# Kernel tuning notes

Hardware: AMD Instinct MI355X
Metric: run time of the kernel (lower is better)

The kernel has to match this reference:

```python
import jax, jax.numpy as jnp
import numpy as np

B, S, N = 16, 512, 321          # batch, input length, n_variates (dec_in)
D, DF, LAYERS = 512, 2048, 2    # d_model, d_ff, e_layers
M, K, P = 3, 3, 96              # wavelet levels, kernel_size, pred_len
ALPHA = 0.3


def _dwconv(x, h, dilation):
    # x: [B, C, L], h: [C, K] depthwise dilated conv (cross-correlation, like torch)
    return jax.lax.conv_general_dilated(
        x, h[:, None, :], window_strides=(1,), padding='VALID',
        rhs_dilation=(dilation,), dimension_numbers=('NCH', 'OIH', 'NCH'),
        feature_group_count=x.shape[1])


def _swt_dec(x, h0, h1):
    # stationary wavelet decomposition; x: [B, N, D] -> [B, N, M+1, D]
    approx, coeffs, dil = x, [], 1
    for _ in range(M):
        pad_total = dil * (K - 1)
        pad_r = (K * dil) // 2
        xp = jnp.pad(approx, ((0, 0), (0, 0), (pad_total - pad_r, pad_r)), mode='wrap')
        coeffs.append(_dwconv(xp, h1, dil))
        approx = _dwconv(xp, h0, dil)
        dil *= 2
    coeffs.append(approx)
    return jnp.stack(coeffs[::-1], axis=-2)


def _swt_rec(c, g0, g1):
    # inverse SWT; c: [B, N, M+1, D] -> [B, N, D]
    approx = c[:, :, 0, :]
    dil = 2 ** (M - 1)
    for i in range(M):
        det = c[:, :, 1 + i, :]
        pad_total = dil * (K - 1)
        pad_l = (dil * K) // 2
        pads = ((0, 0), (0, 0), (pad_l, pad_total - pad_l))
        approx = (_dwconv(jnp.pad(approx, pads, mode='wrap'), g0, dil)
                  + _dwconv(jnp.pad(det, pads, mode='wrap'), g1, dil)) / 2
        dil //= 2
    return approx


def _geom_attention(q, k, v):
    # q,k,v: [B, L=D, H=M+1, E=N]
    scale = 1.0 / jnp.sqrt(jnp.float32(q.shape[-1]))
    dot = jnp.einsum('blhe,bshe->bhls', q, k)
    qn2 = jnp.sum(q * q, -1).transpose(0, 2, 1)  # [B,H,L]
    kn2 = jnp.sum(k * k, -1).transpose(0, 2, 1)  # [B,H,S]
    wedge = jnp.sqrt(jax.nn.relu(qn2[:, :, :, None] * kn2[:, :, None, :] - dot * dot) + 1e-8)
    scores = ((1.0 - ALPHA) * dot + ALPHA * wedge) * scale
    A = jax.nn.softmax(scores, axis=-1)
    return jnp.einsum('bhls,bshd->blhd', A, v)


def _layernorm(x, g, b, eps=1e-5):
    mu = x.mean(-1, keepdims=True)
    var = jnp.mean((x - mu) ** 2, -1, keepdims=True)
    return (x - mu) / jnp.sqrt(var + eps) * g + b


def _forward(x_enc, emb_W, emb_b, h0, h1, g0, g1, Wq, bq, Wk, bk, Wv, bv, Wo, bo,
             W1, b1, W2, b2, ln1_g, ln1_b, ln2_g, ln2_b, lnf_g, lnf_b, proj_W, proj_b):
    # RevIN-style normalize (means detached as in torch code)
    means = jax.lax.stop_gradient(x_enc.mean(1, keepdims=True))
    stdev = jnp.sqrt(x_enc.var(1, keepdims=True) + 1e-5)
    x = (x_enc - means) / stdev
    # inverted embedding: each variate's full series -> d_model token
    h = jnp.einsum('bsn,ds->bnd', x, emb_W) + emb_b  # [B,N,D]
    for l in range(LAYERS):
        coeffs = _swt_dec(h, h0[l], h1[l])  # [B,N,M+1,D]
        q = (jnp.einsum('bnmd,ed->bnme', coeffs, Wq[l]) + bq[l]).transpose(0, 3, 2, 1)
        kk = (jnp.einsum('bnmd,ed->bnme', coeffs, Wk[l]) + bk[l]).transpose(0, 3, 2, 1)
        vv = (jnp.einsum('bnmd,ed->bnme', coeffs, Wv[l]) + bv[l]).transpose(0, 3, 2, 1)
        out = _geom_attention(q, kk, vv).transpose(0, 3, 2, 1)  # [B,N,M+1,D]
        out = _swt_rec(out, g0[l], g1[l])                        # [B,N,D]
        out = jnp.einsum('bnd,ed->bne', out, Wo[l]) + bo[l]
        x1 = _layernorm(h + out, ln1_g[l], ln1_b[l])
        y = jax.nn.gelu(jnp.einsum('bnd,fd->bnf', x1, W1[l]) + b1[l], approximate=False)
        y = jnp.einsum('bnf,df->bnd', y, W2[l]) + b2[l]
        h = _layernorm(x1 + y, ln2_g[l], ln2_b[l])
    h = _layernorm(h, lnf_g, lnf_b)
    dec = (jnp.einsum('bnd,pd->bnp', h, proj_W) + proj_b).transpose(0, 2, 1)  # [B,P,N]
    dec = dec * stdev[:, 0, :][:, None, :] + means[:, 0, :][:, None, :]
    return dec, means, stdev


def setup_inputs():
    key = jax.random.key(0)
    ks = jax.random.split(key, 24)
    def filt(k):
        f = jax.random.normal(k, (LAYERS, N, K), jnp.float32)
        return f / jnp.linalg.norm(f, axis=-1, keepdims=True)
    w = lambda k, shape: jax.random.normal(k, shape, jnp.float32) * 0.02
    z = lambda shape: jnp.zeros(shape, jnp.float32)
    o = lambda shape: jnp.ones(shape, jnp.float32)
    return {
        'x_enc': jax.random.normal(ks[0], (B, S, N), jnp.float32),
        'emb_W': w(ks[1], (D, S)), 'emb_b': z((D,)),
        'h0': filt(ks[2]), 'h1': filt(ks[3]), 'g0': filt(ks[4]), 'g1': filt(ks[5]),
        'Wq': w(ks[6], (LAYERS, D, D)), 'bq': z((LAYERS, D)),
        'Wk': w(ks[7], (LAYERS, D, D)), 'bk': z((LAYERS, D)),
        'Wv': w(ks[8], (LAYERS, D, D)), 'bv': z((LAYERS, D)),
        'Wo': w(ks[9], (LAYERS, D, D)), 'bo': z((LAYERS, D)),
        'W1': w(ks[10], (LAYERS, DF, D)), 'b1': z((LAYERS, DF)),
        'W2': w(ks[11], (LAYERS, D, DF)), 'b2': z((LAYERS, D)),
        'ln1_g': o((LAYERS, D)), 'ln1_b': z((LAYERS, D)),
        'ln2_g': o((LAYERS, D)), 'ln2_b': z((LAYERS, D)),
        'lnf_g': o((D,)), 'lnf_b': z((D,)),
        'proj_W': w(ks[12], (P, D)), 'proj_b': z((P,)),
    }


def reference(x_enc, emb_W, emb_b, h0, h1, g0, g1, Wq, bq, Wk, bk, Wv, bv, Wo, bo,
              W1, b1, W2, b2, ln1_g, ln1_b, ln2_g, ln2_b, lnf_g, lnf_b, proj_W, proj_b):
    return _forward(x_enc, emb_W, emb_b, h0, h1, g0, g1, Wq, bq, Wk, bk, Wv, bv, Wo, bo,
                    W1, b1, W2, b2, ln1_g, ln1_b, ln2_g, ln2_b, lnf_g, lnf_b, proj_W, proj_b)
```

## Files before the change

kernel.cpp:

```cpp
#include <hip/hip_runtime.h>
#include <hip/hip_bf16.h>
#include <math.h>
#include <stdint.h>

#define Bn 16
#define Sn 512
#define Nn 321
#define Dn 512
#define DFn 2048
#define Pn 96
#define KP 352

typedef __bf16 bf16x8 __attribute__((ext_vector_type(8)));
typedef float f32x4 __attribute__((ext_vector_type(4)));
typedef __hip_bfloat16 bf16;

static __device__ __forceinline__ float gelu_exact(float x) {
    return 0.5f * x * (1.0f + erff(x * 0.7071067811865476f));
}

static __device__ __forceinline__ void gld16(const void* g, void* l) {
    __builtin_amdgcn_global_load_lds(
        (const __attribute__((address_space(1))) void*)(uintptr_t)g,
        (__attribute__((address_space(3))) void*)(uintptr_t)l, 16, 0, 0);
}

struct CvtPack {
    const float* src[14];
    bf16* dst[14];
    int cnt[14];
};
__global__ void cvt_all_kernel(CvtPack p) {
    int seg = blockIdx.y;
    int n = p.cnt[seg];
    const float* s = p.src[seg];
    bf16* d = p.dst[seg];
    int i = (blockIdx.x * 256 + threadIdx.x) * 4;
    if (i + 3 < n) {
        float4 v = *reinterpret_cast<const float4*>(s + i);
        d[i] = __float2bfloat16(v.x);
        d[i + 1] = __float2bfloat16(v.y);
        d[i + 2] = __float2bfloat16(v.z);
        d[i + 3] = __float2bfloat16(v.w);
    }
}

__global__ void bias_pack_kernel(const float* __restrict__ bq, const float* __restrict__ bk,
                                 float* __restrict__ bqk) {
    int idx = blockIdx.x * 256 + threadIdx.x;
    if (idx >= 2048) return;
    int l = idx >> 10, j = idx & 1023;
    bqk[idx] = (j < 512) ? bq[l * 512 + j] : bk[l * 512 + j - 512];
}

__global__ void stats_kernel(const float* __restrict__ x, float* __restrict__ means,
                             float* __restrict__ stdev) {
    int b = blockIdx.y;
    int n = blockIdx.x * 256 + threadIdx.x;
    if (n >= Nn) return;
    const float* p = x + (size_t)b * Sn * Nn + n;
    float s = 0.f, s2 = 0.f;
    for (int ss = 0; ss < Sn; ++ss) { float v = p[(size_t)ss * Nn]; s += v; s2 += v * v; }
    float mu = s * (1.0f / Sn);
    float var = s2 * (1.0f / Sn) - mu * mu;
    means[b * Nn + n] = mu;
    stdev[b * Nn + n] = sqrtf(var + 1e-5f);
}

__global__ void transpose_norm_kernel(const float* __restrict__ x,
                                      const float* __restrict__ means,
                                      const float* __restrict__ stdev,
                                      bf16* __restrict__ xT) {
    __shared__ float tile[32][33];
    int b = blockIdx.z;
    int s0 = blockIdx.x * 32, n0 = blockIdx.y * 32;
    int tx = threadIdx.x, ty = threadIdx.y;
#pragma unroll
    for (int u = 0; u < 4; ++u) {
        int srow = ty + u * 8;
        int n = n0 + tx;
        tile[srow][tx] = (n < Nn) ? x[((size_t)b * Sn + (s0 + srow)) * Nn + n] : 0.f;
    }
    __syncthreads();
#pragma unroll
    for (int u = 0; u < 4; ++u) {
        int n = n0 + ty + u * 8;
        int s = s0 + tx;
        if (n < Nn) {
            float mu = means[b * Nn + n], sd = stdev[b * Nn + n];
            xT[((size_t)b * Nn + n) * Sn + s] = __float2bfloat16((tile[tx][ty + u * 8] - mu) / sd);
        }
    }
}

template <int OUT, int EPI>
__global__ __launch_bounds__(256) void mm_kernel(
    const bf16* __restrict__ A, const bf16* __restrict__ Bm,
    const float* __restrict__ bias, void* __restrict__ C,
    int Mdim, int Ndim, int Kdim, int lda, int ldb, int ldc,
    long sAi, long sAo, long sBi, long sBo, long sCi, long sCo, int innerB) {
    int z = blockIdx.z;
    int zi = z % innerB, zo = z / innerB;
    const bf16* Ab = A + (size_t)zi * sAi + (size_t)zo * sAo;
    const bf16* Bb = Bm + (size_t)zi * sBi + (size_t)zo * sBo;

    int gx = gridDim.x, gy = gridDim.y;
    int lin = blockIdx.y * gx + blockIdx.x;
    int prefix = (gy & ~7) * gx;
    int bx, by;
    if (lin < prefix) {
        bx = (lin >> 3) % gx;
        by = (lin / (8 * gx)) * 8 + (lin & 7);
    } else {
        int r = lin - prefix;
        bx = r % gx;
        by = (gy & ~7) + r / gx;
    }

    __shared__ __align__(16) bf16 As[2][128 * 32];
    __shared__ __align__(16) bf16 Bs[2][128 * 32];
    int t = threadIdx.x;
    int wave = t >> 6, lane = t & 63;
    int wr = wave >> 1, wc = wave & 1;
    int q = lane >> 4, l16 = lane & 15;
    int i0 = by * 128, j0 = bx * 128;

    int srow0 = t >> 2;
    int scol = (t & 3) * 8;
    f32x4 acc[4][4] = {};

    int nIter = Kdim >> 5;

    auto stage = [&](int k0, int buf) {
#pragma unroll
        for (int u = 0; u < 2; ++u) {
            int row = u * 64 + srow0;
            int gcol = scol ^ (((row >> 1) & 3) << 3);
            int gi = i0 + row; if (gi >= Mdim) gi = Mdim - 1;
            gld16(Ab + (size_t)gi * lda + k0 + gcol, &As[buf][u * 2048 + wave * 512]);
            int gj = j0 + row; if (gj >= Ndim) gj = Ndim - 1;
            gld16(Bb + (size_t)gj * ldb + k0 + gcol, &Bs[buf][u * 2048 + wave * 512]);
        }
    };

    stage(0, 0);
    for (int it = 0; it < nIter; ++it) {
        __syncthreads();
        if (it + 1 < nIter) stage((it + 1) << 5, (it + 1) & 1);
        int buf = it & 1;
        bf16x8 af[4], bfr[4];
#pragma unroll
        for (int mi = 0; mi < 4; ++mi) {
            int r = wr * 64 + mi * 16 + l16;
            int cl = (q * 8) ^ (((r >> 1) & 3) << 3);
            af[mi] = *reinterpret_cast<const bf16x8*>(&As[buf][r * 32 + cl]);
        }
#pragma unroll
        for (int ni = 0; ni < 4; ++ni) {
            int r = wc * 64 + ni * 16 + l16;
            int cl = (q * 8) ^ (((r >> 1) & 3) << 3);
            bfr[ni] = *reinterpret_cast<const bf16x8*>(&Bs[buf][r * 32 + cl]);
        }
#pragma unroll
        for (int mi = 0; mi < 4; ++mi)
#pragma unroll
            for (int ni = 0; ni < 4; ++ni)
                acc[mi][ni] = __builtin_amdgcn_mfma_f32_16x16x32_bf16(af[mi], bfr[ni], acc[mi][ni], 0, 0, 0);
    }
    size_t cbase = (size_t)zi * sCi + (size_t)zo * sCo;
#pragma unroll
    for (int mi = 0; mi < 4; ++mi) {
#pragma unroll
        for (int r = 0; r < 4; ++r) {
            int gi = i0 + wr * 64 + mi * 16 + q * 4 + r;
            if (gi >= Mdim) continue;
#pragma unroll
            for (int ni = 0; ni < 4; ++ni) {
                int gj = j0 + wc * 64 + ni * 16 + l16;
                if (gj >= Ndim) continue;
                float v = acc[mi][ni][r];
                if (bias) v += bias[gj];
                if (EPI == 1) v = gelu_exact(v);
                size_t cidx = cbase + (size_t)gi * ldc + gj;
                if (OUT == 0) ((float*)C)[cidx] = v;
                else ((bf16*)C)[cidx] = __float2bfloat16(v);
            }
        }
    }
}

__global__ __launch_bounds__(128) void swt_dec_kernel(
    const float* __restrict__ h, const float* __restrict__ h0f,
    const float* __restrict__ h1f, bf16* __restrict__ coeffs) {
    __shared__ float a[2][512];
    int b = blockIdx.y, n = blockIdx.x, t = threadIdx.x;
    const float* hrow = h + ((size_t)b * Nn + n) * Dn;
#pragma unroll
    for (int u = 0; u < 4; ++u) a[0][t + u * 128] = hrow[t + u * 128];
    float f0[3], f1[3];
#pragma unroll
    for (int k = 0; k < 3; ++k) { f0[k] = h0f[n * 3 + k]; f1[k] = h1f[n * 3 + k]; }
    __syncthreads();
    bf16* cb = coeffs + ((size_t)b * Nn + n) * 4 * Dn;
    int cur = 0;
    for (int lev = 0; lev < 3; ++lev) {
        int dil = 1 << lev;
        int pl = 2 * dil - (3 * dil) / 2;
#pragma unroll
        for (int u = 0; u < 4; ++u) {
            int d = t + u * 128;
            float dv = 0.f, av = 0.f;
#pragma unroll
            for (int k = 0; k < 3; ++k) {
                int idx = (d + k * dil - pl) & 511;
                float xv = a[cur][idx];
                dv += f1[k] * xv;
                av += f0[k] * xv;
            }
            cb[(size_t)(3 - lev) * Dn + d] = __float2bfloat16(dv);
            a[cur ^ 1][d] = av;
        }
        __syncthreads();
        cur ^= 1;
    }
#pragma unroll
    for (int u = 0; u < 4; ++u) cb[t + u * 128] = __float2bfloat16(a[cur][t + u * 128]);
}

__global__ __launch_bounds__(128) void swt_rec_kernel(
    const bf16* __restrict__ attn, const float* __restrict__ g0f,
    const float* __restrict__ g1f, bf16* __restrict__ rec) {
    __shared__ float a[2][512];
    __shared__ float det[512];
    int b = blockIdx.y, n = blockIdx.x, t = threadIdx.x;
    const bf16* base = attn + ((size_t)(b * 4) * Nn + n) * Dn;
#pragma unroll
    for (int u = 0; u < 4; ++u) a[0][t + u * 128] = __bfloat162float(base[t + u * 128]);
    float w0[3], w1[3];
#pragma unroll
    for (int k = 0; k < 3; ++k) { w0[k] = g0f[n * 3 + k]; w1[k] = g1f[n * 3 + k]; }
    int cur = 0;
    for (int i = 0; i < 3; ++i) {
        int dil = 4 >> i;
        int pl = (3 * dil) / 2;
        const bf16* drow = base + (size_t)(1 + i) * Nn * Dn;
#pragma unroll
        for (int u = 0; u < 4; ++u) det[t + u * 128] = __bfloat162float(drow[t + u * 128]);
        __syncthreads();
#pragma unroll
        for (int u = 0; u < 4; ++u) {
            int d = t + u * 128;
            float s = 0.f;
#pragma unroll
            for (int k = 0; k < 3; ++k) {
                int idx = (d + k * dil - pl) & 511;
                s += w0[k] * a[cur][idx] + w1[k] * det[idx];
            }
            a[cur ^ 1][d] = s * 0.5f;
        }
        __syncthreads();
        cur ^= 1;
    }
    bf16* out = rec + ((size_t)b * Nn + n) * Dn;
#pragma unroll
    for (int u = 0; u < 4; ++u) out[t + u * 128] = __float2bfloat16(a[cur][t + u * 128]);
}

__global__ void tconv2_kernel(const bf16* __restrict__ QK, bf16* __restrict__ QtKt) {
    __shared__ bf16 tile[32][33];
    int zz = blockIdx.z;
    int qk = zz >> 6, bm = zz & 63;
    int b = bm >> 2, m = bm & 3;
    int e0 = blockIdx.x * 32, n0 = blockIdx.y * 32;
    int tx = threadIdx.x, ty = threadIdx.y;
    const bf16* ib = QK + (size_t)b * Nn * 4096 + (size_t)m * 1024 + (size_t)qk * 512;
    bf16* ob = QtKt + (size_t)qk * 64 * 512 * KP + (size_t)bm * 512 * KP;
#pragma unroll
    for (int u = 0; u < 4; ++u) {
        int n = n0 + ty + u * 8;
        bf16 v = __float2bfloat16(0.f);
        if (n < Nn) v = ib[(size_t)n * 4096 + e0 + tx];
        tile[ty + u * 8][tx] = v;
    }
    __syncthreads();
#pragma unroll
    for (int u = 0; u < 4; ++u) {
        int e = e0 + ty + u * 8;
        int n = n0 + tx;
        if (n < KP) ob[(size_t)e * KP + n] = tile[tx][ty + u * 8];
    }
}

__global__ __launch_bounds__(256) void colsq_t_kernel(const bf16* __restrict__ QtKt,
                                                      float* __restrict__ outv) {
    int wave = threadIdx.x >> 6, lane = threadIdx.x & 63;
    size_t row = (size_t)blockIdx.x * 4 + wave;
    const bf16* p = QtKt + row * KP;
    float s = 0.f;
#pragma unroll
    for (int j = 0; j < 6; ++j) {
        int idx = lane + j * 64;
        if (idx < KP) { float v = __bfloat162float(p[idx]); s += v * v; }
    }
#pragma unroll
    for (int m = 1; m < 64; m <<= 1) s += __shfl_xor(s, m);
    if (lane == 0) outv[row] = s;
}

__global__ __launch_bounds__(256) void wedge_softmax_kernel(
    bf16* __restrict__ Smat, const float* __restrict__ qn2, const float* __restrict__ kn2) {
    int wave = threadIdx.x >> 6, lane = threadIdx.x & 63;
    int rowid = blockIdx.x * 4 + wave;
    int bm = rowid >> 9, l = rowid & 511;
    bf16* row = Smat + (size_t)rowid * 512;
    const float* kn = kn2 + (size_t)bm * 512;
    float q2 = qn2[(size_t)bm * 512 + l];
    const float scale = rsqrtf(321.0f);
    bf16x8 dv = *reinterpret_cast<const bf16x8*>(row + lane * 8);
    float kk[8];
    *reinterpret_cast<float4*>(&kk[0]) = *reinterpret_cast<const float4*>(kn + lane * 8);
    *reinterpret_cast<float4*>(&kk[4]) = *reinterpret_cast<const float4*>(kn + lane * 8 + 4);
    float sc[8];
    float mx = -1e30f;
#pragma unroll
    for (int j = 0; j < 8; ++j) {
        float d = (float)dv[j];
        float w = sqrtf(fmaxf(q2 * kk[j] - d * d, 0.f) + 1e-8f);
        sc[j] = (0.7f * d + 0.3f * w) * scale;
        mx = fmaxf(mx, sc[j]);
    }
#pragma unroll
    for (int m = 1; m < 64; m <<= 1) mx = fmaxf(mx, __shfl_xor(mx, m));
    float sum = 0.f;
#pragma unroll
    for (int j = 0; j < 8; ++j) { sc[j] = expf(sc[j] - mx); sum += sc[j]; }
#pragma unroll
    for (int m = 1; m < 64; m <<= 1) sum += __shfl_xor(sum, m);
    float inv = 1.0f / sum;
    bf16x8 o;
#pragma unroll
    for (int j = 0; j < 8; ++j) o[j] = (__bf16)(sc[j] * inv);
    *reinterpret_cast<bf16x8*>(row + lane * 8) = o;
}

__global__ __launch_bounds__(256) void ln_kernel(
    const float* __restrict__ A, const float* __restrict__ R, const float* __restrict__ R2,
    const float* __restrict__ g, const float* __restrict__ bb,
    float* __restrict__ outf, bf16* __restrict__ outb) {
    int wave = threadIdx.x >> 6, lane = threadIdx.x & 63;
    size_t r = (size_t)blockIdx.x * 4 + wave;
    const float* ra = A + r * Dn + lane * 8;
    float x[8];
    *reinterpret_cast<float4*>(&x[0]) = *reinterpret_cast<const float4*>(ra);
    *reinterpret_cast<float4*>(&x[4]) = *reinterpret_cast<const float4*>(ra + 4);
    if (R) {
        const float* rr = R + r * Dn + lane * 8;
        float y[8];
        *reinterpret_cast<float4*>(&y[0]) = *reinterpret_cast<const float4*>(rr);
        *reinterpret_cast<float4*>(&y[4]) = *reinterpret_cast<const float4*>(rr + 4);
#pragma unroll
        for (int j = 0; j < 8; ++j) x[j] += y[j];
    }
    if (R2) {
        const float* rr = R2 + r * Dn + lane * 8;
        float y[8];
        *reinterpret_cast<float4*>(&y[0]) = *reinterpret_cast<const float4*>(rr);
        *reinterpret_cast<float4*>(&y[4]) = *reinterpret_cast<const float4*>(rr + 4);
#pragma unroll
        for (int j = 0; j < 8; ++j) x[j] += y[j];
    }
    float s = 0.f, s2 = 0.f;
#pragma unroll
    for (int j = 0; j < 8; ++j) { s += x[j]; s2 += x[j] * x[j]; }
#pragma unroll
    for (int m = 1; m < 64; m <<= 1) { s += __shfl_xor(s, m); s2 += __shfl_xor(s2, m); }
    float mean = s * (1.0f / Dn);
    float var = s2 * (1.0f / Dn) - mean * mean;
    float inv = rsqrtf(var + 1e-5f);
#pragma unroll
    for (int j = 0; j < 8; ++j) {
        int d = lane * 8 + j;
        float v = (x[j] - mean) * inv * g[d] + bb[d];
        if (outf) outf[r * Dn + d] = v;
        if (outb) outb[r * Dn + d] = __float2bfloat16(v);
    }
}

__global__ void out_scale_kernel(const float* __restrict__ ptmp,
                                 const float* __restrict__ means,
                                 const float* __restrict__ stdev, float* __restrict__ dec) {
    int idx = blockIdx.x * 256 + threadIdx.x;
    if (idx >= Bn * Pn * Nn) return;
    int n = idx % Nn;
    int bp = idx / Nn;
    int p = bp % Pn;
    int b = bp / Pn;
    const size_t PS = (size_t)Bn * Nn * Pn;
    size_t base = ((size_t)b * Nn + n) * Pn + p;
    float v = ptmp[base] + ptmp[base + PS] + ptmp[base + 2 * PS] + ptmp[base + 3 * PS];
    dec[idx] = v * stdev[b * Nn + n] + means[b * Nn + n];
}

extern "C" void kernel_launch(void* const* d_in, const int* in_sizes, int n_in,
                              void* d_out, int out_size, void* d_ws, size_t ws_size,
                              hipStream_t stream) {
    const float* x_enc = (const float*)d_in[0];
    const float* emb_W = (const float*)d_in[1];
    const float* emb_b = (const float*)d_in[2];
    const float* h0 = (const float*)d_in[3];
    const float* h1 = (const float*)d_in[4];
    const float* g0 = (const float*)d_in[5];
    const float* g1 = (const float*)d_in[6];
    const float* Wq = (const float*)d_in[7];
    const float* bq = (const float*)d_in[8];
    const float* Wk = (const float*)d_in[9];
    const float* bk = (const float*)d_in[10];
    const float* Wv = (const float*)d_in[11];
    const float* bv = (const float*)d_in[12];
    const float* Wo = (const float*)d_in[13];
    const float* bo = (const float*)d_in[14];
    const float* W1 = (const float*)d_in[15];
    const float* b1 = (const float*)d_in[16];
    const float* W2 = (const float*)d_in[17];
    const float* b2 = (const float*)d_in[18];
    const float* ln1_g = (const float*)d_in[19];
    const float* ln1_b = (const float*)d_in[20];
    const float* ln2_g = (const float*)d_in[21];
    const float* ln2_b = (const float*)d_in[22];
    const float* lnf_g = (const float*)d_in[23];
    const float* lnf_b = (const float*)d_in[24];
    const float* proj_W = (const float*)d_in[25];
    const float* proj_b = (const float*)d_in[26];

    float* dec = (float*)d_out;
    float* means = dec + (size_t)Bn * Pn * Nn;
    float* stdev = means + (size_t)Bn * Nn;

    char* p = (char*)d_ws;
    auto alloc = [&](size_t bytes) { char* r = p; p += (bytes + 255) & ~(size_t)255; return r; };
    const size_t RD = (size_t)Bn * Nn * Dn;
    const size_t RQ4 = RD * 4;

    bf16* embWb = (bf16*)alloc(262144 * 2);
    bf16* Wqkb = (bf16*)alloc(2 * 524288 * 2);
    bf16* Wvb = (bf16*)alloc(2 * 262144 * 2);
    bf16* Wob = (bf16*)alloc(2 * 262144 * 2);
    bf16* W1b = (bf16*)alloc(2 * 1048576 * 2);
    bf16* W2b = (bf16*)alloc(2 * 1048576 * 2);
    bf16* projWb = (bf16*)alloc(49152 * 2);
    float* bqk = (float*)alloc(2048 * 4);

    float* hbuf = (float*)alloc(RD * 4);
    char* regC = alloc(RQ4 * 2);
    char* regQ = alloc(RQ4 * 2);
    char* regK = alloc(RQ4 * 2);
    char* regV = alloc(RQ4 * 2);
    char* regT = alloc((size_t)2 * 64 * 512 * KP * 2);
    float* qn2 = (float*)alloc((size_t)2 * 64 * 512 * 4);
    float* kn2 = qn2 + 32768;

    bf16* coeffs_b = (bf16*)regC;
    bf16* attn_b = (bf16*)regC;
    bf16* QK0b = (bf16*)regQ;
    bf16* Smat = (bf16*)regQ;
    bf16* recb = (bf16*)regQ;
    bf16* x1b = (bf16*)(regQ + RD * 2);
    float* ptmp = (float*)regQ;
    bf16* V0b = (bf16*)regV;
    bf16* yb = (bf16*)regV;
    bf16* QtKt = (bf16*)regT;
    bf16* Qt = QtKt;
    bf16* Kt = QtKt + (size_t)64 * 512 * KP;
    bf16* xT_b = (bf16*)regT;
    float* x1 = (float*)regT;
    float* tmp = (float*)(regT + RD * 4);
    bf16* hfb = (bf16*)(regT + RD * 12);

    const int R = Bn * Nn;
    const int RQr = R * 4;
    const long sbm = (long)4 * Nn * 512;
    const long sS = (long)512 * 512;
    const long sTq = (long)512 * KP;
    const long sTb = 4 * sTq;

    CvtPack cp;
    int ci = 0;
    auto addcvt = [&](const float* s, bf16* d, int n) { cp.src[ci] = s; cp.dst[ci] = d; cp.cnt[ci] = n; ++ci; };
    addcvt(emb_W, embWb, 262144);
    for (int l = 0; l < 2; ++l) {
        addcvt(Wq + (size_t)l * 262144, Wqkb + (size_t)l * 524288, 262144);
        addcvt(Wk + (size_t)l * 262144, Wqkb + (size_t)l * 524288 + 262144, 262144);
        addcvt(Wv + (size_t)l * 262144, Wvb + (size_t)l * 262144, 262144);
        addcvt(Wo + (size_t)l * 262144, Wob + (size_t)l * 262144, 262144);
        addcvt(W1 + (size_t)l * 1048576, W1b + (size_t)l * 1048576, 1048576);
        addcvt(W2 + (size_t)l * 1048576, W2b + (size_t)l * 1048576, 1048576);
    }
    addcvt(proj_W, projWb, 49152);
    cvt_all_kernel<<<dim3(1048576 / 4 / 256, 14), 256, 0, stream>>>(cp);
    bias_pack_kernel<<<8, 256, 0, stream>>>(bq, bk, bqk);

    stats_kernel<<<dim3((Nn + 255) / 256, Bn), 256, 0, stream>>>(x_enc, means, stdev);
    transpose_norm_kernel<<<dim3(Sn / 32, (Nn + 31) / 32, Bn), dim3(32, 8), 0, stream>>>(
        x_enc, means, stdev, xT_b);

    mm_kernel<0, 0><<<dim3(4, (R + 127) / 128, 1), 256, 0, stream>>>(
        xT_b, embWb, emb_b, hbuf, R, Dn, Sn, Sn, Sn, Dn, 0, 0, 0, 0, 0, 0, 1);

    for (int l = 0; l < 2; ++l) {
        const float* h0l = h0 + (size_t)l * Nn * 3;
        const float* h1l = h1 + (size_t)l * Nn * 3;
        const float* g0l = g0 + (size_t)l * Nn * 3;
        const float* g1l = g1 + (size_t)l * Nn * 3;

        swt_dec_kernel<<<dim3(Nn, Bn), 128, 0, stream>>>(hbuf, h0l, h1l, coeffs_b);

        mm_kernel<1, 0><<<dim3(8, (RQr + 127) / 128, 1), 256, 0, stream>>>(
            coeffs_b, Wqkb + (size_t)l * 524288, bqk + (size_t)l * 1024, QK0b,
            RQr, 1024, Dn, Dn, Dn, 1024, 0, 0, 0, 0, 0, 0, 1);
        mm_kernel<1, 0><<<dim3(4, (RQr + 127) / 128, 1), 256, 0, stream>>>(
            coeffs_b, Wvb + (size_t)l * 262144, bv + (size_t)l * Dn, V0b,
            RQr, Dn, Dn, Dn, Dn, Dn, 0, 0, 0, 0, 0, 0, 1);

        tconv2_kernel<<<dim3(16, 11, 128), dim3(32, 8), 0, stream>>>(QK0b, QtKt);
        colsq_t_kernel<<<16384, 256, 0, stream>>>(QtKt, qn2);

        mm_kernel<1, 0><<<dim3(4, 4, 64), 256, 0, stream>>>(
            Qt, Kt, nullptr, Smat, 512, 512, KP, KP, KP, 512,
            sTq, sTb, sTq, sTb, sS, 4 * sS, 4);

        wedge_softmax_kernel<<<8192, 256, 0, stream>>>(Smat, qn2, kn2);

        mm_kernel<1, 0><<<dim3(4, (Nn + 127) / 128, 64), 256, 0, stream>>>(
            V0b, Smat, nullptr, attn_b, Nn, 512, 512, 2048, 512, 512,
            512, sbm, sS, 4 * sS, (long)Nn * 512, (long)4 * Nn * 512, 4);

        swt_rec_kernel<<<dim3(Nn, Bn), 128, 0, stream>>>(attn_b, g0l, g1l, recb);

        mm_kernel<0, 0><<<dim3(4, (R + 127) / 128, 2), 256, 0, stream>>>(
            recb, Wob + (size_t)l * 262144, bo + (size_t)l * Dn, tmp,
            R, Dn, 256, Dn, Dn, Dn, 256, 0, 256, 0, (long)RD, 0, 2);
        ln_kernel<<<R / 4, 256, 0, stream>>>(hbuf, tmp, tmp + RD, ln1_g + (size_t)l * Dn,
                                             ln1_b + (size_t)l * Dn, x1, x1b);

        mm_kernel<1, 1><<<dim3(16, (R + 127) / 128, 1), 256, 0, stream>>>(
            x1b, W1b + (size_t)l * 1048576, b1 + (size_t)l * DFn, yb,
            R, DFn, Dn, Dn, Dn, DFn, 0, 0, 0, 0, 0, 0, 1);
        mm_kernel<0, 0><<<dim3(4, (R + 127) / 128, 2), 256, 0, stream>>>(
            yb, W2b + (size_t)l * 1048576, b2 + (size_t)l * Dn, tmp,
            R, Dn, 1024, DFn, DFn, Dn, 1024, 0, 1024, 0, (long)RD, 0, 2);
        ln_kernel<<<R / 4, 256, 0, stream>>>(x1, tmp, tmp + RD, ln2_g + (size_t)l * Dn,
                                             ln2_b + (size_t)l * Dn, hbuf, nullptr);
    }

    ln_kernel<<<R / 4, 256, 0, stream>>>(hbuf, nullptr, nullptr, lnf_g, lnf_b, nullptr, hfb);
    mm_kernel<0, 0><<<dim3(1, (R + 127) / 128, 4), 256, 0, stream>>>(
        hfb, projWb, proj_b, ptmp, R, Pn, 128, Dn, Dn, Pn,
        128, 0, 128, 0, (long)R * Pn, 0, 4);
    out_scale_kernel<<<(Bn * Pn * Nn + 255) / 256, 256, 0, stream>>>(ptmp, means, stdev, dec);
}
```

Baseline: 906.8 us.

## Fuse Q/K/V projections into one GEMM and split-K the embedding GEMM

Packs the Wq, Wk and Wv weights and their biases into one matrix, so one GEMM with N=1536 reads the wavelet coefficients once. Its epilogue routes columns at or above 1024 to the separate V buffer. The embedding GEMM becomes a two-way split-K writing partials to tmp, and the first layer's SWT decomposition kernel sums those partials and writes hbuf. The aim is to cut kernel launches, reread the A operand less often and give the small embedding GEMM more parallelism, at the cost of an extra fp32 partial write and read.

```diff
diff --git a/kernel.cpp b/kernel.cpp
--- a/kernel.cpp
+++ b/kernel.cpp
@@ -46,11 +46,13 @@
 }
 
 __global__ void bias_pack_kernel(const float* __restrict__ bq, const float* __restrict__ bk,
-                                 float* __restrict__ bqk) {
+                                 const float* __restrict__ bv, float* __restrict__ bqkv) {
     int idx = blockIdx.x * 256 + threadIdx.x;
-    if (idx >= 2048) return;
-    int l = idx >> 10, j = idx & 1023;
-    bqk[idx] = (j < 512) ? bq[l * 512 + j] : bk[l * 512 + j - 512];
+    if (idx >= 3072) return;
+    int l = idx / 1536, j = idx % 1536;
+    float v = (j < 512) ? bq[l * 512 + j]
+            : (j < 1024 ? bk[l * 512 + j - 512] : bv[l * 512 + j - 1024]);
+    bqkv[idx] = v;
 }
 
 __global__ void stats_kernel(const float* __restrict__ x, float* __restrict__ means,
@@ -93,10 +95,10 @@
     }
 }
 
-template <int OUT, int EPI>
+template <int OUT, int EPI, int DUAL>
 __global__ __launch_bounds__(256) void mm_kernel(
     const bf16* __restrict__ A, const bf16* __restrict__ Bm,
-    const float* __restrict__ bias, void* __restrict__ C,
+    const float* __restrict__ bias, void* __restrict__ C, void* __restrict__ C2,
     int Mdim, int Ndim, int Kdim, int lda, int ldb, int ldc,
     long sAi, long sAo, long sBi, long sBo, long sCi, long sCo, int innerB) {
     int z = blockIdx.z;
@@ -181,27 +183,37 @@
                 float v = acc[mi][ni][r];
                 if (bias) v += bias[gj];
                 if (EPI == 1) v = gelu_exact(v);
-                size_t cidx = cbase + (size_t)gi * ldc + gj;
-                if (OUT == 0) ((float*)C)[cidx] = v;
-                else ((bf16*)C)[cidx] = __float2bfloat16(v);
+                if (DUAL && gj >= 1024) {
+                    ((bf16*)C2)[(size_t)gi * 512 + (gj - 1024)] = __float2bfloat16(v);
+                } else {
+                    size_t cidx = cbase + (size_t)gi * ldc + gj;
+                    if (OUT == 0) ((float*)C)[cidx] = v;
+                    else ((bf16*)C)[cidx] = __float2bfloat16(v);
+                }
             }
         }
     }
 }
 
 __global__ __launch_bounds__(128) void swt_dec_kernel(
-    const float* __restrict__ h, const float* __restrict__ h0f,
-    const float* __restrict__ h1f, bf16* __restrict__ coeffs) {
+    const float* __restrict__ h, const float* __restrict__ h2, float* __restrict__ hout,
+    const float* __restrict__ h0f, const float* __restrict__ h1f, bf16* __restrict__ coeffs) {
     __shared__ float a[2][512];
     int b = blockIdx.y, n = blockIdx.x, t = threadIdx.x;
-    const float* hrow = h + ((size_t)b * Nn + n) * Dn;
-#pragma unroll
-    for (int u = 0; u < 4; ++u) a[0][t + u * 128] = hrow[t + u * 128];
+    size_t roff = ((size_t)b * Nn + n) * Dn;
+    const float* hrow = h + roff;
+#pragma unroll
+    for (int u = 0; u < 4; ++u) {
+        float v = hrow[t + u * 128];
+        if (h2) v += h2[roff + t + u * 128];
+        a[0][t + u * 128] = v;
+        if (hout) hout[roff + t + u * 128] = v;
+    }
     float f0[3], f1[3];
 #pragma unroll
     for (int k = 0; k < 3; ++k) { f0[k] = h0f[n * 3 + k]; f1[k] = h1f[n * 3 + k]; }
     __syncthreads();
-    bf16* cb = coeffs + ((size_t)b * Nn + n) * 4 * Dn;
+    bf16* cb = coeffs + roff * 4;
     int cur = 0;
     for (int lev = 0; lev < 3; ++lev) {
         int dil = 1 << lev;
@@ -442,13 +454,12 @@
     const size_t RQ4 = RD * 4;
 
     bf16* embWb = (bf16*)alloc(262144 * 2);
-    bf16* Wqkb = (bf16*)alloc(2 * 524288 * 2);
-    bf16* Wvb = (bf16*)alloc(2 * 262144 * 2);
+    bf16* Wqkvb = (bf16*)alloc(2 * 786432 * 2);
     bf16* Wob = (bf16*)alloc(2 * 262144 * 2);
     bf16* W1b = (bf16*)alloc(2 * 1048576 * 2);
     bf16* W2b = (bf16*)alloc(2 * 1048576 * 2);
     bf16* projWb = (bf16*)alloc(49152 * 2);
-    float* bqk = (float*)alloc(2048 * 4);
+    float* bqkv = (float*)alloc(3072 * 4);
 
     float* hbuf = (float*)alloc(RD * 4);
     char* regC = alloc(RQ4 * 2);
@@ -488,23 +499,24 @@
     auto addcvt = [&](const float* s, bf16* d, int n) { cp.src[ci] = s; cp.dst[ci] = d; cp.cnt[ci] = n; ++ci; };
     addcvt(emb_W, embWb, 262144);
     for (int l = 0; l < 2; ++l) {
-        addcvt(Wq + (size_t)l * 262144, Wqkb + (size_t)l * 524288, 262144);
-        addcvt(Wk + (size_t)l * 262144, Wqkb + (size_t)l * 524288 + 262144, 262144);
-        addcvt(Wv + (size_t)l * 262144, Wvb + (size_t)l * 262144, 262144);
+        addcvt(Wq + (size_t)l * 262144, Wqkvb + (size_t)l * 786432, 262144);
+        addcvt(Wk + (size_t)l * 262144, Wqkvb + (size_t)l * 786432 + 262144, 262144);
+        addcvt(Wv + (size_t)l * 262144, Wqkvb + (size_t)l * 786432 + 524288, 262144);
         addcvt(Wo + (size_t)l * 262144, Wob + (size_t)l * 262144, 262144);
         addcvt(W1 + (size_t)l * 1048576, W1b + (size_t)l * 1048576, 1048576);
         addcvt(W2 + (size_t)l * 1048576, W2b + (size_t)l * 1048576, 1048576);
     }
     addcvt(proj_W, projWb, 49152);
     cvt_all_kernel<<<dim3(1048576 / 4 / 256, 14), 256, 0, stream>>>(cp);
-    bias_pack_kernel<<<8, 256, 0, stream>>>(bq, bk, bqk);
+    bias_pack_kernel<<<12, 256, 0, stream>>>(bq, bk, bv, bqkv);
 
     stats_kernel<<<dim3((Nn + 255) / 256, Bn), 256, 0, stream>>>(x_enc, means, stdev);
     transpose_norm_kernel<<<dim3(Sn / 32, (Nn + 31) / 32, Bn), dim3(32, 8), 0, stream>>>(
         x_enc, means, stdev, xT_b);
 
-    mm_kernel<0, 0><<<dim3(4, (R + 127) / 128, 1), 256, 0, stream>>>(
-        xT_b, embWb, emb_b, hbuf, R, Dn, Sn, Sn, Sn, Dn, 0, 0, 0, 0, 0, 0, 1);
+    mm_kernel<0, 0, 0><<<dim3(4, (R + 127) / 128, 2), 256, 0, stream>>>(
+        xT_b, embWb, emb_b, tmp, nullptr, R, Dn, 256, Sn, Sn, Dn,
+        256, 0, 256, 0, (long)RD, 0, 2);
 
     for (int l = 0; l < 2; ++l) {
         const float* h0l = h0 + (size_t)l * Nn * 3;
@@ -512,49 +524,49 @@
         const float* g0l = g0 + (size_t)l * Nn * 3;
         const float* g1l = g1 + (size_t)l * Nn * 3;
 
-        swt_dec_kernel<<<dim3(Nn, Bn), 128, 0, stream>>>(hbuf, h0l, h1l, coeffs_b);
-
-        mm_kernel<1, 0><<<dim3(8, (RQr + 127) / 128, 1), 256, 0, stream>>>(
-            coeffs_b, Wqkb + (size_t)l * 524288, bqk + (size_t)l * 1024, QK0b,
-            RQr, 1024, Dn, Dn, Dn, 1024, 0, 0, 0, 0, 0, 0, 1);
-        mm_kernel<1, 0><<<dim3(4, (RQr + 127) / 128, 1), 256, 0, stream>>>(
-            coeffs_b, Wvb + (size_t)l * 262144, bv + (size_t)l * Dn, V0b,
-            RQr, Dn, Dn, Dn, Dn, Dn, 0, 0, 0, 0, 0, 0, 1);
+        if (l == 0)
+            swt_dec_kernel<<<dim3(Nn, Bn), 128, 0, stream>>>(tmp, tmp + RD, hbuf, h0l, h1l, coeffs_b);
+        else
+            swt_dec_kernel<<<dim3(Nn, Bn), 128, 0, stream>>>(hbuf, nullptr, nullptr, h0l, h1l, coeffs_b);
+
+        mm_kernel<1, 0, 1><<<dim3(12, (RQr + 127) / 128, 1), 256, 0, stream>>>(
+            coeffs_b, Wqkvb + (size_t)l * 786432, bqkv + (size_t)l * 1536, QK0b, V0b,
+            RQr, 1536, Dn, Dn, Dn, 1024, 0, 0, 0, 0, 0, 0, 1);
 
         tconv2_kernel<<<dim3(16, 11, 128), dim3(32, 8), 0, stream>>>(QK0b, QtKt);
         colsq_t_kernel<<<16384, 256, 0, stream>>>(QtKt, qn2);
 
-        mm_kernel<1, 0><<<dim3(4, 4, 64), 256, 0, stream>>>(
-            Qt, Kt, nullptr, Smat, 512, 512, KP, KP, KP, 512,
+        mm_kernel<1, 0, 0><<<dim3(4, 4, 64), 256, 0, stream>>>(
+            Qt, Kt, nullptr, Smat, nullptr, 512, 512, KP, KP, KP, 512,
             sTq, sTb, sTq, sTb, sS, 4 * sS, 4);
 
         wedge_softmax_kernel<<<8192, 256, 0, stream>>>(Smat, qn2, kn2);
 
-        mm_kernel<1, 0><<<dim3(4, (Nn + 127) / 128, 64), 256, 0, stream>>>(
-            V0b, Smat, nullptr, attn_b, Nn, 512, 512, 2048, 512, 512,
+        mm_kernel<1, 0, 0><<<dim3(4, (Nn + 127) / 128, 64), 256, 0, stream>>>(
+            V0b, Smat, nullptr, attn_b, nullptr, Nn, 512, 512, 2048, 512, 512,
             512, sbm, sS, 4 * sS, (long)Nn * 512, (long)4 * Nn * 512, 4);
 
         swt_rec_kernel<<<dim3(Nn, Bn), 128, 0, stream>>>(attn_b, g0l, g1l, recb);
 
-        mm_kernel<0, 0><<<dim3(4, (R + 127) / 128, 2), 256, 0, stream>>>(
-            recb, Wob + (size_t)l * 262144, bo + (size_t)l * Dn, tmp,
+        mm_kernel<0, 0, 0><<<dim3(4, (R + 127) / 128, 2), 256, 0, stream>>>(
+            recb, Wob + (size_t)l * 262144, bo + (size_t)l * Dn, tmp, nullptr,
             R, Dn, 256, Dn, Dn, Dn, 256, 0, 256, 0, (long)RD, 0, 2);
         ln_kernel<<<R / 4, 256, 0, stream>>>(hbuf, tmp, tmp + RD, ln1_g + (size_t)l * Dn,
                                              ln1_b + (size_t)l * Dn, x1, x1b);
 
-        mm_kernel<1, 1><<<dim3(16, (R + 127) / 128, 1), 256, 0, stream>>>(
-            x1b, W1b + (size_t)l * 1048576, b1 + (size_t)l * DFn, yb,
+        mm_kernel<1, 1, 0><<<dim3(16, (R + 127) / 128, 1), 256, 0, stream>>>(
+            x1b, W1b + (size_t)l * 1048576, b1 + (size_t)l * DFn, yb, nullptr,
             R, DFn, Dn, Dn, Dn, DFn, 0, 0, 0, 0, 0, 0, 1);
-        mm_kernel<0, 0><<<dim3(4, (R + 127) / 128, 2), 256, 0, stream>>>(
-            yb, W2b + (size_t)l * 1048576, b2 + (size_t)l * Dn, tmp,
+        mm_kernel<0, 0, 0><<<dim3(4, (R + 127) / 128, 2), 256, 0, stream>>>(
+            yb, W2b + (size_t)l * 1048576, b2 + (size_t)l * Dn, tmp, nullptr,
             R, Dn, 1024, DFn, DFn, Dn, 1024, 0, 1024, 0, (long)RD, 0, 2);
         ln_kernel<<<R / 4, 256, 0, stream>>>(x1, tmp, tmp + RD, ln2_g + (size_t)l * Dn,
                                              ln2_b + (size_t)l * Dn, hbuf, nullptr);
     }
 
     ln_kernel<<<R / 4, 256, 0, stream>>>(hbuf, nullptr, nullptr, lnf_g, lnf_b, nullptr, hfb);
-    mm_kernel<0, 0><<<dim3(1, (R + 127) / 128, 4), 256, 0, stream>>>(
-        hfb, projWb, proj_b, ptmp, R, Pn, 128, Dn, Dn, Pn,
+    mm_kernel<0, 0, 0><<<dim3(1, (R + 127) / 128, 4), 256, 0, stream>>>(
+        hfb, projWb, proj_b, ptmp, nullptr, R, Pn, 128, Dn, Dn, Pn,
         128, 0, 128, 0, (long)R * Pn, 0, 4);
     out_scale_kernel<<<(Bn * Pn * Nn + 255) / 256, 256, 0, stream>>>(ptmp, means, stdev, dec);
 }
```

New measurement: 989.3 us. 9.1% more time.
